# Performance work log

Hardware: AMD Instinct MI355X
Metric: run time of the kernel (lower is better)

Reference implementation:

```python
import jax, jax.numpy as jnp
import numpy as np

NUM_SAMPLED_POINTS = 512
POOL_EXTRA_WIDTH = 1.0


def setup_inputs() -> dict:
    key = jax.random.key(0)
    k1, k2, k3, k4, k5 = jax.random.split(key, 5)
    B, N, C, M = 4, 16384, 128, 128
    points = jax.random.normal(k1, (B, N, 3), dtype=jnp.float32) * 2.0
    point_features = jax.random.normal(k2, (B, N, C), dtype=jnp.float32)
    centers = jax.random.normal(k3, (B, M, 3), dtype=jnp.float32) * 2.0
    sizes = jax.random.uniform(k4, (B, M, 3), dtype=jnp.float32, minval=1.0, maxval=3.0)
    yaw = jax.random.uniform(k5, (B, M, 1), dtype=jnp.float32, minval=0.0, maxval=2.0 * np.pi)
    boxes3d = jnp.concatenate([centers, sizes, yaw], axis=-1)  # (B, M, 7)
    return {"points": points, "point_features": point_features, "boxes3d": boxes3d}


def _enlarge_box3d(boxes3d, extra_width):
    # (x, y, z_bottom, dx, dy, dz, yaw): grow sizes, lower bottom by extra_width/2
    delta = jnp.array([0.0, 0.0, -extra_width / 2.0,
                       extra_width, extra_width, extra_width, 0.0], dtype=boxes3d.dtype)
    return boxes3d + delta


def reference(points, point_features, boxes3d):
    B, N, _ = points.shape
    M = boxes3d.shape[1]
    S = NUM_SAMPLED_POINTS

    big = _enlarge_box3d(boxes3d, POOL_EXTRA_WIDTH)  # (B, M, 7)
    cx, cy, cz = big[..., 0:1], big[..., 1:2], big[..., 2:3]   # (B, M, 1)
    dx, dy, dz = big[..., 3:4], big[..., 4:5], big[..., 5:6]
    yaw = big[..., 6:7]

    px = points[:, None, :, 0]  # (B, 1, N) -> broadcast to (B, M, N)
    py = points[:, None, :, 1]
    pz = points[:, None, :, 2]

    # rotate into box frame (rotate by -yaw around z)
    cosa, sina = jnp.cos(yaw), jnp.sin(yaw)
    sx, sy = px - cx, py - cy
    local_x = sx * cosa + sy * sina
    local_y = -sx * sina + sy * cosa
    in_box = (jnp.abs(local_x) < dx * 0.5) & (jnp.abs(local_y) < dy * 0.5) \
             & (jnp.abs(pz - (cz + dz * 0.5)) <= dz * 0.5)  # (B, M, N)

    cnt = in_box.sum(axis=-1).astype(jnp.int32)  # (B, M)
    # inside points first, preserving original point order
    order = jnp.argsort(jnp.logical_not(in_box), axis=-1, stable=True)  # (B, M, N)

    k = jnp.arange(S, dtype=jnp.int32)  # (S,)
    cnt_safe = jnp.maximum(cnt, 1)[..., None]  # (B, M, 1)
    # slot k takes the k-th inside point; if cnt < S, wrap: k % cnt
    r = jnp.where(k[None, None, :] < cnt[..., None], k[None, None, :], k[None, None, :] % cnt_safe)
    idx = jnp.take_along_axis(order, r, axis=-1)  # (B, M, S)

    pts_feat = jnp.concatenate([points, point_features], axis=-1)  # (B, N, 3 + C)
    gathered = jnp.take_along_axis(pts_feat[:, None, :, :], idx[..., None], axis=2)  # (B, M, S, 3+C)

    empty = (cnt == 0)
    pooled_features = jnp.where(empty[..., None, None], jnp.zeros((), gathered.dtype), gathered)
    pooled_empty_flag = empty.astype(jnp.int32)
    return pooled_features, pooled_empty_flag
```

## Files before the change

### kernel.cpp

```cpp
#include <hip/hip_runtime.h>
#include <math.h>

#define BB 4
#define NN 16384
#define CC 128
#define MM 128
#define SS 512
#define OUT_ROW 131
#define NSEG 256
#define ELEMS_PER_BOX (SS * OUT_ROW)
#define G2 16
#define RPG2 32
#define TILE2_F4 (RPG2 * OUT_ROW / 4)

typedef float f32x4 __attribute__((ext_vector_type(4)));

__global__ __launch_bounds__(512) void k1_select(
    const float* __restrict__ points,
    const float* __restrict__ boxes,
    int* __restrict__ ws_idx,
    int* __restrict__ ws_cnt,
    float* __restrict__ out_flag)
{
    const int bm   = blockIdx.x;
    const int b    = bm >> 7;
    const int m    = bm & (MM - 1);
    const int tid  = threadIdx.x;
    const int lane = tid & 63;
    const int wave = tid >> 6;

    __shared__ unsigned long long s_mask[NSEG];
    __shared__ int s_wsum[4];

    const float* bx = boxes + (size_t)(b * MM + m) * 7;
    const float cx  = bx[0];
    const float cy  = bx[1];
    const float cz  = __fadd_rn(bx[2], -0.5f);
    const float hx  = __fmul_rn(__fadd_rn(bx[3], 1.0f), 0.5f);
    const float hy  = __fmul_rn(__fadd_rn(bx[4], 1.0f), 0.5f);
    const float hz  = __fmul_rn(__fadd_rn(bx[5], 1.0f), 0.5f);
    const float yaw = bx[6];
    const float cosa = (float)cos((double)yaw);
    const float sina = (float)sin((double)yaw);
    const float zc   = __fadd_rn(cz, hz);

    const float* pbase = points + (size_t)b * NN * 3;

    #pragma unroll 4
    for (int k = 0; k < 32; ++k) {
        const int s = wave * 32 + k;
        const int i = s * 64 + lane;
        const float px = pbase[i * 3 + 0];
        const float py = pbase[i * 3 + 1];
        const float pz = pbase[i * 3 + 2];
        const float sx = __fadd_rn(px, -cx);
        const float sy = __fadd_rn(py, -cy);
        const float lx = __fadd_rn(__fmul_rn(sx, cosa), __fmul_rn(sy, sina));
        const float ly = __fadd_rn(__fmul_rn(-sx, sina), __fmul_rn(sy, cosa));
        const bool in_box = (fabsf(lx) < hx) & (fabsf(ly) < hy) &
                            (fabsf(__fadd_rn(pz, -zc)) <= hz);
        const unsigned long long mask = __ballot(in_box);
        if (lane == 0) s_mask[s] = mask;
    }
    __syncthreads();

    unsigned long long mymask = 0ull;
    int c = 0;
    if (tid < NSEG) {
        mymask = s_mask[tid];
        c = __popcll(mymask);
    }
    int inc = c;
    #pragma unroll
    for (int d = 1; d < 64; d <<= 1) {
        int v = __shfl_up(inc, d);
        if (lane >= d) inc += v;
    }
    if (tid < NSEG && lane == 63) s_wsum[wave] = inc;
    __syncthreads();

    int woff = 0, total = 0;
    #pragma unroll
    for (int w = 0; w < 4; ++w) {
        const int v = s_wsum[w];
        if (w < wave) woff += v;
        total += v;
    }

    int* dst = ws_idx + (size_t)bm * SS;

    if (tid < NSEG) {
        int base = woff + inc - c;
        if (base < SS) {
            unsigned long long mk = mymask;
            while (mk) {
                const int bit = __ffsll(mk) - 1;
                mk &= mk - 1;
                dst[base] = tid * 64 + bit;
                if (++base >= SS) break;
            }
        }
    }
    __syncthreads();

    const int cnt = total;
    if (cnt > 0) {
        for (int row = cnt + tid; row < SS; row += 512)
            dst[row] = dst[row % cnt];
    }
    if (tid == 0) {
        ws_cnt[bm] = cnt;
        out_flag[bm] = (cnt == 0) ? 1.0f : 0.0f;
    }
}

__global__ __launch_bounds__(256) void k2_gather(
    const float* __restrict__ points,
    const float* __restrict__ feats,
    const int* __restrict__ ws_idx,
    const int* __restrict__ ws_cnt,
    float* __restrict__ out_feat)
{
    const int orig = blockIdx.x;
    const int blk  = ((orig & 7) << 10) | (orig >> 3);
    const int bm   = blk >> 4;
    const int g    = blk & (G2 - 1);
    const int row0 = g << 5;
    const int tid  = threadIdx.x;

    const int cnt = ws_cnt[bm];
    float* oreg = out_feat + (size_t)bm * ELEMS_PER_BOX + (size_t)row0 * OUT_ROW;

    if (cnt == 0) {
        const f32x4 z = (f32x4)0.0f;
        for (int e4 = tid; e4 < TILE2_F4; e4 += 256)
            __builtin_nontemporal_store(z, (f32x4*)oreg + e4);
        return;
    }

    __shared__ float s_tile[RPG2 * OUT_ROW];

    const int b = bm >> 7;
    const float* pb = points + (size_t)b * NN * 3;
    const float* fb = feats + (size_t)b * NN * CC;
    const int lane = tid & 63;
    const int wave = tid >> 6;
    const int half = lane >> 5;
    const int sl   = lane & 31;
    const int* idx = ws_idx + (size_t)bm * SS + row0;

    const int idxreg = idx[lane & 31];

    if (tid < RPG2 * 3) {
        const int row = tid / 3, c = tid - row * 3;
        s_tile[row * OUT_ROW + c] = pb[idx[row] * 3 + c];
    }

    #pragma unroll
    for (int p = 0; p < 4; ++p) {
        const int row = p * 8 + wave * 2 + half;
        const int pi  = __shfl(idxreg, row);
        const f32x4 v = *(const f32x4*)(fb + (size_t)pi * CC + sl * 4);
        float* d = &s_tile[row * OUT_ROW + 3 + sl * 4];
        d[0] = v.x; d[1] = v.y; d[2] = v.z; d[3] = v.w;
    }
    __syncthreads();

    for (int e4 = tid; e4 < TILE2_F4; e4 += 256) {
        const int e = e4 * 4;
        f32x4 v;
        v.x = s_tile[e + 0]; v.y = s_tile[e + 1];
        v.z = s_tile[e + 2]; v.w = s_tile[e + 3];
        __builtin_nontemporal_store(v, (f32x4*)oreg + e4);
    }
}

extern "C" void kernel_launch(void* const* d_in, const int* in_sizes, int n_in,
                              void* d_out, int out_size, void* d_ws, size_t ws_size,
                              hipStream_t stream) {
    const float* points = (const float*)d_in[0];
    const float* feats  = (const float*)d_in[1];
    const float* boxes  = (const float*)d_in[2];
    float* out_feat = (float*)d_out;
    float* out_flag = (float*)d_out + (size_t)BB * MM * SS * OUT_ROW;

    int* ws_idx = (int*)d_ws;
    int* ws_cnt = ws_idx + (size_t)BB * MM * SS;

    k1_select<<<BB * MM, 512, 0, stream>>>(points, boxes, ws_idx, ws_cnt, out_flag);
    k2_gather<<<BB * MM * G2, 256, 0, stream>>>(points, feats, ws_idx, ws_cnt, out_feat);
}
```

Before: 48.62 us.

## Gather directly into output-aligned float4 registers, bypassing LDS tile staging

The gather kernel no longer stages each 32-row tile in shared memory. Each thread now works out which output float4 it owns, loads the matching 16 bytes straight from the feature row (unaligned memcpy), and falls back to per-element loads where a float4 spans the xyz columns or a row boundary. All loads are issued before the nontemporal stores, which removes the LDS round trip and one barrier. The cost is unaligned global loads, some divergent scalar paths, and integer division by 131 per element.

```diff
diff --git a/kernel.cpp b/kernel.cpp
--- a/kernel.cpp
+++ b/kernel.cpp
@@ -10,8 +10,7 @@
 #define NSEG 256
 #define ELEMS_PER_BOX (SS * OUT_ROW)
 #define G2 16
-#define RPG2 32
-#define TILE2_F4 (RPG2 * OUT_ROW / 4)
+#define QPB 1048
 
 typedef float f32x4 __attribute__((ext_vector_type(4)));
 
@@ -129,49 +128,64 @@
     const int tid  = threadIdx.x;
 
     const int cnt = ws_cnt[bm];
-    float* oreg = out_feat + (size_t)bm * ELEMS_PER_BOX + (size_t)row0 * OUT_ROW;
+    f32x4* oq = (f32x4*)(out_feat + (size_t)bm * ELEMS_PER_BOX
+                                  + (size_t)row0 * OUT_ROW);
 
     if (cnt == 0) {
         const f32x4 z = (f32x4)0.0f;
-        for (int e4 = tid; e4 < TILE2_F4; e4 += 256)
-            __builtin_nontemporal_store(z, (f32x4*)oreg + e4);
+        #pragma unroll
+        for (int it = 0; it < 5; ++it) {
+            const int e4 = tid + it * 256;
+            if (it == 4 && tid >= QPB - 1024) continue;
+            __builtin_nontemporal_store(z, oq + e4);
+        }
         return;
     }
 
-    __shared__ float s_tile[RPG2 * OUT_ROW];
+    __shared__ int s_pi[33];
+    if (tid < 33) {
+        int r = row0 + tid; if (r > SS - 1) r = SS - 1;
+        s_pi[tid] = ws_idx[(size_t)bm * SS + r];
+    }
+    __syncthreads();
 
     const int b = bm >> 7;
     const float* pb = points + (size_t)b * NN * 3;
     const float* fb = feats + (size_t)b * NN * CC;
-    const int lane = tid & 63;
-    const int wave = tid >> 6;
-    const int half = lane >> 5;
-    const int sl   = lane & 31;
-    const int* idx = ws_idx + (size_t)bm * SS + row0;
-
-    const int idxreg = idx[lane & 31];
-
-    if (tid < RPG2 * 3) {
-        const int row = tid / 3, c = tid - row * 3;
-        s_tile[row * OUT_ROW + c] = pb[idx[row] * 3 + c];
-    }
-
-    #pragma unroll
-    for (int p = 0; p < 4; ++p) {
-        const int row = p * 8 + wave * 2 + half;
-        const int pi  = __shfl(idxreg, row);
-        const f32x4 v = *(const f32x4*)(fb + (size_t)pi * CC + sl * 4);
-        float* d = &s_tile[row * OUT_ROW + 3 + sl * 4];
-        d[0] = v.x; d[1] = v.y; d[2] = v.z; d[3] = v.w;
-    }
-    __syncthreads();
-
-    for (int e4 = tid; e4 < TILE2_F4; e4 += 256) {
-        const int e = e4 * 4;
-        f32x4 v;
-        v.x = s_tile[e + 0]; v.y = s_tile[e + 1];
-        v.z = s_tile[e + 2]; v.w = s_tile[e + 3];
-        __builtin_nontemporal_store(v, (f32x4*)oreg + e4);
+
+    f32x4 vv[5];
+    #pragma unroll
+    for (int it = 0; it < 5; ++it) {
+        const int e4 = tid + it * 256;
+        if (it == 4 && tid >= QPB - 1024) continue;
+        const int e   = e4 * 4;
+        const int rl  = e / 131;
+        const int col = e - rl * 131;
+        if (col >= 3 && col <= 127) {
+            const int pi = s_pi[rl];
+            f32x4 v;
+            __builtin_memcpy(&v, fb + (size_t)pi * CC + (col - 3), 16);
+            vv[it] = v;
+        } else {
+            f32x4 v;
+            #pragma unroll
+            for (int j = 0; j < 4; ++j) {
+                const int gg    = col + j;
+                const int cross = (gg >= OUT_ROW) ? 1 : 0;
+                const int rl2   = rl + cross;
+                const int c2    = gg - cross * OUT_ROW;
+                const int pi2   = s_pi[rl2];
+                v[j] = (c2 < 3) ? pb[pi2 * 3 + c2]
+                                : fb[(size_t)pi2 * CC + (c2 - 3)];
+            }
+            vv[it] = v;
+        }
+    }
+    #pragma unroll
+    for (int it = 0; it < 5; ++it) {
+        const int e4 = tid + it * 256;
+        if (it == 4 && tid >= QPB - 1024) continue;
+        __builtin_nontemporal_store(vv[it], oq + e4);
     }
 }
 
```

Measured after the change: 49.20 us. Within noise of the previous version (+1.2%).
